# Kernel optimization log

Measured on AMD Instinct MI355X. Metric: run time of the kernel, lower is better.

The kernel has to match this reference:

```python
import jax, jax.numpy as jnp
import numpy as np

N_NODES = 50000
N_EDGES = 800000
D_IN = 128
HIDDEN = 128
N_GRAPHS = 64


def gcn_conv(x, src, dst, W, b, num_nodes):
    """PyG GCNConv: out = D^{-1/2} (A+I) D^{-1/2} (x W) + b.
    src/dst already include self-loops."""
    h = x @ W  # [N, out]
    deg = jax.ops.segment_sum(jnp.ones_like(dst, dtype=h.dtype), dst,
                              num_segments=num_nodes)  # in-degree incl. self loop
    dinv = jnp.where(deg > 0, jax.lax.rsqrt(jnp.maximum(deg, 1e-12)), 0.0)
    norm = dinv[src] * dinv[dst]  # [E+N]
    msgs = h[src] * norm[:, None]  # gather + scale
    out = jax.ops.segment_sum(msgs, dst, num_segments=num_nodes)
    return out + b


def setup_inputs() -> dict:
    key = jax.random.key(0)
    ks = jax.random.split(key, 8)
    x = jax.random.normal(ks[0], (N_NODES, D_IN), dtype=jnp.float32)
    edge_index = jax.random.randint(ks[1], (2, N_EDGES), 0, N_NODES, dtype=jnp.int64)
    batch = jnp.sort(jax.random.randint(ks[2], (N_NODES,), 0, N_GRAPHS, dtype=jnp.int64))
    # Glorot-ish scaled params
    s = lambda fan_in: 1.0 / np.sqrt(fan_in)
    W1 = jax.random.normal(ks[3], (D_IN, HIDDEN), dtype=jnp.float32) * s(D_IN)
    b1 = jnp.zeros((HIDDEN,), dtype=jnp.float32)
    W2 = jax.random.normal(ks[4], (HIDDEN, HIDDEN), dtype=jnp.float32) * s(HIDDEN)
    b2 = jnp.zeros((HIDDEN,), dtype=jnp.float32)
    Wh1 = jax.random.normal(ks[5], (HIDDEN, HIDDEN), dtype=jnp.float32) * s(HIDDEN)
    bh1 = jnp.zeros((HIDDEN,), dtype=jnp.float32)
    Wh2 = jax.random.normal(ks[6], (HIDDEN, 1), dtype=jnp.float32) * s(HIDDEN)
    bh2 = jnp.zeros((1,), dtype=jnp.float32)
    return {"x": x, "edge_index": edge_index, "batch": batch,
            "W1": W1, "b1": b1, "W2": W2, "b2": b2,
            "Wh1": Wh1, "bh1": bh1, "Wh2": Wh2, "bh2": bh2}


def reference(x, edge_index, batch, W1, b1, W2, b2, Wh1, bh1, Wh2, bh2):
    n = x.shape[0]
    loop = jnp.arange(n, dtype=edge_index.dtype)
    src = jnp.concatenate([edge_index[0], loop])  # add self-loops once
    dst = jnp.concatenate([edge_index[1], loop])
    h = jax.nn.relu(gcn_conv(x, src, dst, W1, b1, n))
    h = jax.nn.relu(gcn_conv(h, src, dst, W2, b2, n))
    # global mean pool over graphs
    sums = jax.ops.segment_sum(h, batch, num_segments=N_GRAPHS)
    cnts = jax.ops.segment_sum(jnp.ones((n,), dtype=h.dtype), batch,
                               num_segments=N_GRAPHS)
    pooled = sums / jnp.maximum(cnts, 1.0)[:, None]  # [G, HIDDEN]
    # MLP head: Linear -> ReLU -> Linear -> Sigmoid -> squeeze(-1)
    z = jax.nn.relu(pooled @ Wh1 + bh1)
    out = jax.nn.sigmoid(z @ Wh2 + bh2)
    return out[:, 0]  # [G]
```

## Files before the change

kernel.cpp:

```cpp
#include <hip/hip_runtime.h>


#define NB 256
#define NBK 256

typedef __attribute__((ext_vector_type(8))) short bf16x8;
typedef __attribute__((ext_vector_type(4))) float f32x4;
typedef __attribute__((ext_vector_type(2))) float f32x2;

__device__ inline unsigned short f2bf(float f) {
    union { float f; unsigned int u; } c; c.f = f;
    unsigned int u = c.u + (0x7fffu + ((c.u >> 16) & 1u));
    return (unsigned short)(u >> 16);
}
__device__ inline float bf2f(unsigned short b) {
    union { unsigned int u; float f; } c; c.u = ((unsigned int)b) << 16;
    return c.f;
}

__device__ inline unsigned char f2fp8_sw(float f) {
    union { float f; unsigned int u; } c; c.f = f;
    unsigned int s = (c.u >> 24) & 0x80u;
    unsigned int au = c.u & 0x7FFFFFFFu;
    if (au >= 0x3C800000u) {
        if (au > 0x43E00000u) au = 0x43E00000u;
        unsigned int r = au + 0x000FFFFFu + ((au >> 20) & 1u);
        unsigned int e8 = (r >> 23) - 120u;
        unsigned int m8 = (r >> 20) & 7u;
        return (unsigned char)(s | (e8 << 3) | m8);
    }
    float av = c.f < 0.f ? -c.f : c.f;
    unsigned int M = (unsigned int)(av * 512.0f + 0.5f);
    return (unsigned char)(s | M);
}
__device__ inline float fp82f_sw(unsigned int cbyte) {
    unsigned int E = (cbyte >> 3) & 0xFu, M = cbyte & 7u;
    union { unsigned int u; float f; } v;
    v.u = ((E + 120u) << 23) | (M << 20);
    float r = E ? v.f : (float)M * 0.001953125f;
    return (cbyte & 0x80u) ? -r : r;
}

__device__ inline f32x2 fp8x2_f32(unsigned int u) {
#if __has_builtin(__builtin_amdgcn_cvt_pk_f32_fp8)
    return __builtin_amdgcn_cvt_pk_f32_fp8(u, false);
#else
    f32x2 r; r[0] = fp82f_sw(u & 0xFFu); r[1] = fp82f_sw((u >> 8) & 0xFFu);
    return r;
#endif
}
__device__ inline unsigned char f2fp8(float f) {
#if __has_builtin(__builtin_amdgcn_cvt_pk_fp8_f32)
    return (unsigned char)(__builtin_amdgcn_cvt_pk_fp8_f32(f, f, 0, false) & 0xFFu);
#else
    return f2fp8_sw(f);
#endif
}

__global__ __launch_bounds__(256) void k_hist(const int* __restrict__ dst,
                                              int* __restrict__ hist,
                                              float* __restrict__ sums,
                                              float* __restrict__ cnt,
                                              int ne, int chunk) {
    __shared__ int h[NBK];
    int t = threadIdx.x, b = blockIdx.x;
    h[t] = 0;
    int gid = b * 256 + t;
    if (gid < 64 * 128) sums[gid] = 0.0f;
    if (gid < 64) cnt[gid] = 0.0f;
    __syncthreads();
    int e0 = b * chunk, e1 = min(e0 + chunk, ne);
    for (int e = e0 + t; e < e1; e += 256) atomicAdd(&h[dst[e] >> 8], 1);
    __syncthreads();
    hist[b * NBK + t] = h[t];
}

__global__ __launch_bounds__(256) void k_scanb(int* __restrict__ hist,
                                               int* __restrict__ bstart,
                                               int* __restrict__ row_start,
                                               int n, int ne) {
    __shared__ int ps[256];
    int j = threadIdx.x;
    int run = 0;
    for (int i = 0; i < NB; ++i) {
        int t = hist[i * NBK + j];
        hist[i * NBK + j] = run;
        run += t;
    }
    ps[j] = run;
    __syncthreads();
    for (int off = 1; off < 256; off <<= 1) {
        int v = (j >= off) ? ps[j - off] : 0;
        __syncthreads();
        ps[j] += v;
        __syncthreads();
    }
    int excl = ps[j] - run;
    bstart[j] = excl;
    if (j == 255) bstart[256] = ps[255];
    if (j == 0) row_start[n] = ne;
    for (int i = 0; i < NB; ++i) hist[i * NBK + j] += excl;
}

__global__ __launch_bounds__(256) void k_scat(const int* __restrict__ src,
                                              const int* __restrict__ dst,
                                              const int* __restrict__ hist,
                                              unsigned int* __restrict__ ebuf,
                                              int ne, int chunk) {
    __shared__ int cur[NBK];
    int t = threadIdx.x, b = blockIdx.x;
    cur[t] = hist[b * NBK + t];
    __syncthreads();
    int e0 = b * chunk, e1 = min(e0 + chunk, ne);
    for (int e = e0 + t; e < e1; e += 256) {
        int d = dst[e];
        int p = atomicAdd(&cur[d >> 8], 1);
        ebuf[p] = ((unsigned int)(d & 255) << 24) | (unsigned int)src[e];
    }
}

__global__ __launch_bounds__(256) void k_bsort(const unsigned int* __restrict__ ebuf,
                                               const int* __restrict__ bstart,
                                               int* __restrict__ csr,
                                               int* __restrict__ row_start,
                                               float* __restrict__ dinv,
                                               int n) {
    __shared__ int h[NBK];
    __shared__ int sc[NBK];
    int j = threadIdx.x, b = blockIdx.x;
    int s0 = bstart[b], s1 = bstart[b + 1];
    h[j] = 0;
    __syncthreads();
    for (int e = s0 + j; e < s1; e += 256) atomicAdd(&h[ebuf[e] >> 24], 1);
    __syncthreads();
    sc[j] = h[j];
    __syncthreads();
    for (int off = 1; off < 256; off <<= 1) {
        int v = (j >= off) ? sc[j - off] : 0;
        __syncthreads();
        sc[j] += v;
        __syncthreads();
    }
    int excl = sc[j] - h[j];
    int id = b * 256 + j;
    int deg = h[j];
    if (id < n) {
        row_start[id] = s0 + excl;
        dinv[id] = rsqrtf((float)deg + 1.0f);
    }
    __syncthreads();
    h[j] = excl;
    __syncthreads();
    for (int e = s0 + j; e < s1; e += 256) {
        unsigned int pk = ebuf[e];
        int p = atomicAdd(&h[pk >> 24], 1);
        csr[s0 + p] = (int)(pk & 0x00FFFFFFu);
    }
}

__global__ __launch_bounds__(256) void k_castw(const float* __restrict__ W1,
                                               const float* __restrict__ W2,
                                               unsigned short* __restrict__ Wt1,
                                               unsigned short* __restrict__ Wt2) {
    int tid = blockIdx.x * 256 + threadIdx.x;
    int i = tid & 16383;
    int nn = i >> 7, kk = i & 127;
    if (tid < 16384) Wt1[i] = f2bf(W1[kk * 128 + nn]);
    else             Wt2[i] = f2bf(W2[kk * 128 + nn]);
}

template <bool F32IN>
__global__ __launch_bounds__(256) void k_gemm_mfma(const void* __restrict__ Xin,
                                                   const short* __restrict__ Wt,
                                                   unsigned char* __restrict__ Y8,
                                                   int n_rows) {
    int wid = threadIdx.x >> 6;
    int lane = threadIdx.x & 63;
    int r = lane & 15, q = lane >> 4;
    int m0 = blockIdx.x * 64;
    int n0 = wid * 32;

    bf16x8 bfr[2][4];
#pragma unroll
    for (int nt = 0; nt < 2; ++nt)
#pragma unroll
        for (int ks = 0; ks < 4; ++ks)
            bfr[nt][ks] = *(const bf16x8*)(Wt + (size_t)(n0 + nt * 16 + r) * 128 +
                                           ks * 32 + q * 8);

#pragma unroll
    for (int rt = 0; rt < 4; ++rt) {
        int row = m0 + rt * 16 + r;
        int rl = min(row, n_rows - 1);
        f32x4 acc0 = {0.f, 0.f, 0.f, 0.f};
        f32x4 acc1 = {0.f, 0.f, 0.f, 0.f};
#pragma unroll
        for (int ks = 0; ks < 4; ++ks) {
            bf16x8 a;
            if constexpr (F32IN) {
                const float* xr = (const float*)Xin + (size_t)rl * 128 + ks * 32 + q * 8;
                float4 f0 = *(const float4*)xr;
                float4 f1 = *(const float4*)(xr + 4);
                a[0] = (short)f2bf(f0.x); a[1] = (short)f2bf(f0.y);
                a[2] = (short)f2bf(f0.z); a[3] = (short)f2bf(f0.w);
                a[4] = (short)f2bf(f1.x); a[5] = (short)f2bf(f1.y);
                a[6] = (short)f2bf(f1.z); a[7] = (short)f2bf(f1.w);
            } else {
                a = *(const bf16x8*)((const short*)Xin + (size_t)rl * 128 + ks * 32 + q * 8);
            }
            acc0 = __builtin_amdgcn_mfma_f32_16x16x32_bf16(a, bfr[0][ks], acc0, 0, 0, 0);
            acc1 = __builtin_amdgcn_mfma_f32_16x16x32_bf16(a, bfr[1][ks], acc1, 0, 0, 0);
        }
#pragma unroll
        for (int v = 0; v < 4; ++v) {
            int orow = m0 + rt * 16 + q * 4 + v;
            if (orow < n_rows) {
                Y8[(size_t)orow * 128 + n0 + r]      = f2fp8(acc0[v]);
                Y8[(size_t)orow * 128 + n0 + 16 + r] = f2fp8(acc1[v]);
            }
        }
    }
}

__global__ __launch_bounds__(256) void k_agg(const unsigned char* __restrict__ h8,
                                             const float* __restrict__ dinv,
                                             const int* __restrict__ csr,
                                             const int* __restrict__ row_start,
                                             const float* __restrict__ bias,
                                             unsigned short* __restrict__ out,
                                             int n) {
    int node = blockIdx.x * 4 + (threadIdx.x >> 6);
    if (node >= n) return;
    int lane = threadIdx.x & 63;
    const unsigned short* h2 = (const unsigned short*)h8;

    float di = dinv[node];

    f32x2 hv = fp8x2_f32(h2[(size_t)node * 64 + lane]);
    float ax = hv[0] * di * di;
    float ay = hv[1] * di * di;

    int beg = row_start[node];
    int end = row_start[node + 1];
    int deg = end - beg;

    int mysrc = (lane < deg) ? csr[beg + lane] : 0;
    float myw = ((lane < deg) ? dinv[mysrc] : 0.0f) * di;

    int m = min(deg, 64);
    int e = 0;
    for (; e + 4 <= m; e += 4) {
        int s0 = __shfl(mysrc, e);
        int s1 = __shfl(mysrc, e + 1);
        int s2 = __shfl(mysrc, e + 2);
        int s3 = __shfl(mysrc, e + 3);
        float w0 = __shfl(myw, e);
        float w1 = __shfl(myw, e + 1);
        float w2 = __shfl(myw, e + 2);
        float w3 = __shfl(myw, e + 3);
        unsigned int u0 = h2[(size_t)s0 * 64 + lane];
        unsigned int u1 = h2[(size_t)s1 * 64 + lane];
        unsigned int u2 = h2[(size_t)s2 * 64 + lane];
        unsigned int u3 = h2[(size_t)s3 * 64 + lane];
        f32x2 v0 = fp8x2_f32(u0);
        f32x2 v1 = fp8x2_f32(u1);
        f32x2 v2 = fp8x2_f32(u2);
        f32x2 v3 = fp8x2_f32(u3);
        ax += v0[0] * w0;  ay += v0[1] * w0;
        ax += v1[0] * w1;  ay += v1[1] * w1;
        ax += v2[0] * w2;  ay += v2[1] * w2;
        ax += v3[0] * w3;  ay += v3[1] * w3;
    }
    for (; e < m; ++e) {
        int s = __shfl(mysrc, e);
        float w = __shfl(myw, e);
        f32x2 v = fp8x2_f32(h2[(size_t)s * 64 + lane]);
        ax += v[0] * w;
        ay += v[1] * w;
    }
    for (int j = beg + 64; j < end; ++j) {
        int s = csr[j];
        float w = dinv[s] * di;
        f32x2 v = fp8x2_f32(h2[(size_t)s * 64 + lane]);
        ax += v[0] * w;
        ay += v[1] * w;
    }

    float2 bv = ((const float2*)bias)[lane];
    float ox = fmaxf(ax + bv.x, 0.0f);
    float oy = fmaxf(ay + bv.y, 0.0f);
    unsigned int pack = (unsigned int)f2bf(ox) | ((unsigned int)f2bf(oy) << 16);
    ((unsigned int*)out)[(size_t)node * 64 + lane] = pack;
}

#define POOL_CHUNK 64
__global__ __launch_bounds__(128) void k_pool(const unsigned short* __restrict__ h,
                                              const int* __restrict__ batch,
                                              float* __restrict__ sums,
                                              float* __restrict__ cnt, int n) {
    int d = threadIdx.x;
    int c0 = blockIdx.x * POOL_CHUNK;
    if (c0 >= n) return;
    int c1 = min(c0 + POOL_CHUNK, n);
    float acc = 0.f, cc = 0.f;
    int g_cur = batch[c0];
    for (int i = c0; i < c1; ++i) {
        int g = batch[i];
        if (g != g_cur) {
            atomicAdd(&sums[g_cur * 128 + d], acc);
            if (d == 0) atomicAdd(&cnt[g_cur], cc);
            acc = 0.f; cc = 0.f; g_cur = g;
        }
        acc += bf2f(h[(size_t)i * 128 + d]);
        cc += 1.f;
    }
    atomicAdd(&sums[g_cur * 128 + d], acc);
    if (d == 0) atomicAdd(&cnt[g_cur], cc);
}

__global__ __launch_bounds__(128) void k_head(const float* __restrict__ sums,
                                              const float* __restrict__ cnt,
                                              const float* __restrict__ Wh1,
                                              const float* __restrict__ bh1,
                                              const float* __restrict__ Wh2,
                                              const float* __restrict__ bh2,
                                              float* __restrict__ out) {
    int g = blockIdx.x;
    int d = threadIdx.x;
    __shared__ float sp[128];
    __shared__ float red[128];
    float c = fmaxf(cnt[g], 1.0f);
    sp[d] = sums[g * 128 + d] / c;
    __syncthreads();
    float acc = bh1[d];
    for (int k = 0; k < 128; ++k) acc += sp[k] * Wh1[k * 128 + d];
    float z = fmaxf(acc, 0.f);
    red[d] = z * Wh2[d];
    __syncthreads();
    for (int off = 64; off > 0; off >>= 1) {
        if (d < off) red[d] += red[d + off];
        __syncthreads();
    }
    if (d == 0) out[g] = 1.f / (1.f + expf(-(red[0] + bh2[0])));
}

extern "C" void kernel_launch(void* const* d_in, const int* in_sizes, int n_in,
                              void* d_out, int out_size, void* d_ws,
                              size_t ws_size, hipStream_t stream) {
    const float* x    = (const float*)d_in[0];
    const int*   ei   = (const int*)d_in[1];
    const int*   batch= (const int*)d_in[2];
    const float* W1   = (const float*)d_in[3];
    const float* b1   = (const float*)d_in[4];
    const float* W2   = (const float*)d_in[5];
    const float* b2   = (const float*)d_in[6];
    const float* Wh1  = (const float*)d_in[7];
    const float* bh1  = (const float*)d_in[8];
    const float* Wh2  = (const float*)d_in[9];
    const float* bh2  = (const float*)d_in[10];
    float* out = (float*)d_out;

    const int n  = in_sizes[0] / 128;
    const int ne = in_sizes[1] / 2;
    const int* src = ei;
    const int* dst = ei + ne;

    char* p = (char*)d_ws;
    int* hist      = (int*)p;  p += (size_t)NB * NBK * 4;
    int* bstart    = (int*)p;  p += 257 * 4;
    int* row_start = (int*)p;  p += (size_t)(n + 1) * 4;
    float* dinv    = (float*)p; p += (size_t)n * 4;
    unsigned int* ebuf = (unsigned int*)p; p += (size_t)ne * 4;
    int* csr       = (int*)p;  p += (size_t)ne * 4;
    p = (char*)(((uintptr_t)p + 15) & ~(uintptr_t)15);
    unsigned short* Wt1 = (unsigned short*)p; p += 128 * 128 * 2;
    unsigned short* Wt2 = (unsigned short*)p; p += 128 * 128 * 2;
    unsigned char* h8   = (unsigned char*)p; p += (size_t)n * 128;
    p = (char*)(((uintptr_t)p + 15) & ~(uintptr_t)15);
    unsigned short* abf = (unsigned short*)p; p += (size_t)n * 128 * 2;
    p = (char*)(((uintptr_t)p + 15) & ~(uintptr_t)15);
    float* sums = (float*)p;   p += (size_t)64 * 128 * 4;
    float* cnt  = (float*)p;

    int chunk = (ne + NB - 1) / NB;
    int nb_g = (n + 63) / 64;
    int nb_a = (n + 3) / 4;
    int nb_p = (n + POOL_CHUNK - 1) / POOL_CHUNK;

    k_hist<<<NB, 256, 0, stream>>>(dst, hist, sums, cnt, ne, chunk);
    k_scanb<<<1, 256, 0, stream>>>(hist, bstart, row_start, n, ne);
    k_scat<<<NB, 256, 0, stream>>>(src, dst, hist, ebuf, ne, chunk);
    k_bsort<<<256, 256, 0, stream>>>(ebuf, bstart, csr, row_start, dinv, n);

    k_castw<<<128, 256, 0, stream>>>(W1, W2, Wt1, Wt2);

    k_gemm_mfma<true><<<nb_g, 256, 0, stream>>>((const void*)x, (const short*)Wt1, h8, n);
    k_agg<<<nb_a, 256, 0, stream>>>(h8, dinv, csr, row_start, b1, abf, n);

    k_gemm_mfma<false><<<nb_g, 256, 0, stream>>>((const void*)abf, (const short*)Wt2, h8, n);
    k_agg<<<nb_a, 256, 0, stream>>>(h8, dinv, csr, row_start, b2, abf, n);

    k_pool<<<nb_p, 128, 0, stream>>>(abf, batch, sums, cnt, n);
    k_head<<<64, 128, 0, stream>>>(sums, cnt, Wh1, bh1, Wh2, bh2, out);
}
```

Measured before the change: 188.3 us.

## Split fp8 features into two column planes and aggregate each plane separately

The GEMM now writes its fp8 output as two 64-column planes of N×64 bytes instead of row-major N×128. Aggregation runs once per plane, so each pass gathers over a working set half the size, which is meant to fit better in cache. Within a pass, each wavefront processes four edges at once, with 16 lanes per edge each loading 4 bytes, and the partial sums are reduced across lanes with shuffles. The cost is twice as many aggregation launches, a second read of the CSR index data, and extra shuffle and reduction work.

```diff
diff --git a/kernel.cpp b/kernel.cpp
--- a/kernel.cpp
+++ b/kernel.cpp
@@ -41,11 +41,13 @@
     return (cbyte & 0x80u) ? -r : r;
 }
 
+template <bool HI>
 __device__ inline f32x2 fp8x2_f32(unsigned int u) {
 #if __has_builtin(__builtin_amdgcn_cvt_pk_f32_fp8)
-    return __builtin_amdgcn_cvt_pk_f32_fp8(u, false);
+    return __builtin_amdgcn_cvt_pk_f32_fp8(u, HI);
 #else
-    f32x2 r; r[0] = fp82f_sw(u & 0xFFu); r[1] = fp82f_sw((u >> 8) & 0xFFu);
+    unsigned int w = HI ? (u >> 16) : u;
+    f32x2 r; r[0] = fp82f_sw(w & 0xFFu); r[1] = fp82f_sw((w >> 8) & 0xFFu);
     return r;
 #endif
 }
@@ -179,6 +181,8 @@
     int r = lane & 15, q = lane >> 4;
     int m0 = blockIdx.x * 64;
     int n0 = wid * 32;
+    unsigned char* Yp = Y8 + (size_t)(n0 >> 6) * n_rows * 64;
+    int c0 = n0 & 63;
 
     bf16x8 bfr[2][4];
 #pragma unroll
@@ -215,30 +219,33 @@
         for (int v = 0; v < 4; ++v) {
             int orow = m0 + rt * 16 + q * 4 + v;
             if (orow < n_rows) {
-                Y8[(size_t)orow * 128 + n0 + r]      = f2fp8(acc0[v]);
-                Y8[(size_t)orow * 128 + n0 + 16 + r] = f2fp8(acc1[v]);
+                Yp[(size_t)orow * 64 + c0 + r]      = f2fp8(acc0[v]);
+                Yp[(size_t)orow * 64 + c0 + 16 + r] = f2fp8(acc1[v]);
             }
         }
     }
 }
 
-__global__ __launch_bounds__(256) void k_agg(const unsigned char* __restrict__ h8,
-                                             const float* __restrict__ dinv,
-                                             const int* __restrict__ csr,
-                                             const int* __restrict__ row_start,
-                                             const float* __restrict__ bias,
-                                             unsigned short* __restrict__ out,
-                                             int n) {
+__global__ __launch_bounds__(256) void k_aggp(const unsigned char* __restrict__ plane,
+                                              const float* __restrict__ dinv,
+                                              const int* __restrict__ csr,
+                                              const int* __restrict__ row_start,
+                                              const float* __restrict__ bias_ph,
+                                              unsigned short* __restrict__ out,
+                                              int n, int phofs) {
     int node = blockIdx.x * 4 + (threadIdx.x >> 6);
     if (node >= n) return;
     int lane = threadIdx.x & 63;
-    const unsigned short* h2 = (const unsigned short*)h8;
+    int slot = lane >> 4, fi = lane & 15;
+    const unsigned int* hp = (const unsigned int*)plane;
 
     float di = dinv[node];
-
-    f32x2 hv = fp8x2_f32(h2[(size_t)node * 64 + lane]);
-    float ax = hv[0] * di * di;
-    float ay = hv[1] * di * di;
+    float selfw = (slot == 0) ? di * di : 0.0f;
+    unsigned int hu = hp[(size_t)node * 16 + fi];
+    f32x2 p0 = fp8x2_f32<false>(hu);
+    f32x2 p1 = fp8x2_f32<true>(hu);
+    float a0 = p0[0] * selfw, a1 = p0[1] * selfw;
+    float a2 = p1[0] * selfw, a3 = p1[1] * selfw;
 
     int beg = row_start[node];
     int end = row_start[node + 1];
@@ -249,48 +256,54 @@
 
     int m = min(deg, 64);
     int e = 0;
-    for (; e + 4 <= m; e += 4) {
-        int s0 = __shfl(mysrc, e);
-        int s1 = __shfl(mysrc, e + 1);
-        int s2 = __shfl(mysrc, e + 2);
-        int s3 = __shfl(mysrc, e + 3);
-        float w0 = __shfl(myw, e);
-        float w1 = __shfl(myw, e + 1);
-        float w2 = __shfl(myw, e + 2);
-        float w3 = __shfl(myw, e + 3);
-        unsigned int u0 = h2[(size_t)s0 * 64 + lane];
-        unsigned int u1 = h2[(size_t)s1 * 64 + lane];
-        unsigned int u2 = h2[(size_t)s2 * 64 + lane];
-        unsigned int u3 = h2[(size_t)s3 * 64 + lane];
-        f32x2 v0 = fp8x2_f32(u0);
-        f32x2 v1 = fp8x2_f32(u1);
-        f32x2 v2 = fp8x2_f32(u2);
-        f32x2 v3 = fp8x2_f32(u3);
-        ax += v0[0] * w0;  ay += v0[1] * w0;
-        ax += v1[0] * w1;  ay += v1[1] * w1;
-        ax += v2[0] * w2;  ay += v2[1] * w2;
-        ax += v3[0] * w3;  ay += v3[1] * w3;
-    }
-    for (; e < m; ++e) {
-        int s = __shfl(mysrc, e);
-        float w = __shfl(myw, e);
-        f32x2 v = fp8x2_f32(h2[(size_t)s * 64 + lane]);
-        ax += v[0] * w;
-        ay += v[1] * w;
-    }
-    for (int j = beg + 64; j < end; ++j) {
-        int s = csr[j];
-        float w = dinv[s] * di;
-        f32x2 v = fp8x2_f32(h2[(size_t)s * 64 + lane]);
-        ax += v[0] * w;
-        ay += v[1] * w;
-    }
-
-    float2 bv = ((const float2*)bias)[lane];
-    float ox = fmaxf(ax + bv.x, 0.0f);
-    float oy = fmaxf(ay + bv.y, 0.0f);
-    unsigned int pack = (unsigned int)f2bf(ox) | ((unsigned int)f2bf(oy) << 16);
-    ((unsigned int*)out)[(size_t)node * 64 + lane] = pack;
+    for (; e + 8 <= m; e += 8) {
+        int i0 = e + slot, i1 = e + 4 + slot;
+        int s0 = __shfl(mysrc, i0);
+        int s1 = __shfl(mysrc, i1);
+        float w0 = __shfl(myw, i0);
+        float w1 = __shfl(myw, i1);
+        unsigned int u0 = hp[(size_t)s0 * 16 + fi];
+        unsigned int u1 = hp[(size_t)s1 * 16 + fi];
+        f32x2 v00 = fp8x2_f32<false>(u0), v01 = fp8x2_f32<true>(u0);
+        f32x2 v10 = fp8x2_f32<false>(u1), v11 = fp8x2_f32<true>(u1);
+        a0 += v00[0] * w0; a1 += v00[1] * w0; a2 += v01[0] * w0; a3 += v01[1] * w0;
+        a0 += v10[0] * w1; a1 += v10[1] * w1; a2 += v11[0] * w1; a3 += v11[1] * w1;
+    }
+    for (; e < m; e += 4) {
+        int idx = e + slot;
+        int s = __shfl(mysrc, idx & 63);
+        float w = __shfl(myw, idx & 63);
+        if (idx >= m) { s = 0; w = 0.0f; }
+        unsigned int u = hp[(size_t)s * 16 + fi];
+        f32x2 v0 = fp8x2_f32<false>(u), v1 = fp8x2_f32<true>(u);
+        a0 += v0[0] * w; a1 += v0[1] * w; a2 += v1[0] * w; a3 += v1[1] * w;
+    }
+    if (slot == 0) {
+        for (int j = beg + 64; j < end; ++j) {
+            int s = csr[j];
+            float w = dinv[s] * di;
+            unsigned int u = hp[(size_t)s * 16 + fi];
+            f32x2 v0 = fp8x2_f32<false>(u), v1 = fp8x2_f32<true>(u);
+            a0 += v0[0] * w; a1 += v0[1] * w; a2 += v1[0] * w; a3 += v1[1] * w;
+        }
+    }
+
+    a0 += __shfl_xor(a0, 16); a0 += __shfl_xor(a0, 32);
+    a1 += __shfl_xor(a1, 16); a1 += __shfl_xor(a1, 32);
+    a2 += __shfl_xor(a2, 16); a2 += __shfl_xor(a2, 32);
+    a3 += __shfl_xor(a3, 16); a3 += __shfl_xor(a3, 32);
+
+    if (slot == 0) {
+        float4 bv = ((const float4*)bias_ph)[fi];
+        float o0 = fmaxf(a0 + bv.x, 0.0f);
+        float o1 = fmaxf(a1 + bv.y, 0.0f);
+        float o2 = fmaxf(a2 + bv.z, 0.0f);
+        float o3 = fmaxf(a3 + bv.w, 0.0f);
+        uint2 pk;
+        pk.x = (unsigned int)f2bf(o0) | ((unsigned int)f2bf(o1) << 16);
+        pk.y = (unsigned int)f2bf(o2) | ((unsigned int)f2bf(o3) << 16);
+        *(uint2*)(out + (size_t)node * 128 + phofs + fi * 4) = pk;
+    }
 }
 
 #define POOL_CHUNK 64
@@ -386,6 +399,7 @@
     int nb_g = (n + 63) / 64;
     int nb_a = (n + 3) / 4;
     int nb_p = (n + POOL_CHUNK - 1) / POOL_CHUNK;
+    size_t plane = (size_t)n * 64;
 
     k_hist<<<NB, 256, 0, stream>>>(dst, hist, sums, cnt, ne, chunk);
     k_scanb<<<1, 256, 0, stream>>>(hist, bstart, row_start, n, ne);
@@ -395,10 +409,12 @@
     k_castw<<<128, 256, 0, stream>>>(W1, W2, Wt1, Wt2);
 
     k_gemm_mfma<true><<<nb_g, 256, 0, stream>>>((const void*)x, (const short*)Wt1, h8, n);
-    k_agg<<<nb_a, 256, 0, stream>>>(h8, dinv, csr, row_start, b1, abf, n);
+    k_aggp<<<nb_a, 256, 0, stream>>>(h8,         dinv, csr, row_start, b1,      abf, n, 0);
+    k_aggp<<<nb_a, 256, 0, stream>>>(h8 + plane, dinv, csr, row_start, b1 + 64, abf, n, 64);
 
     k_gemm_mfma<false><<<nb_g, 256, 0, stream>>>((const void*)abf, (const short*)Wt2, h8, n);
-    k_agg<<<nb_a, 256, 0, stream>>>(h8, dinv, csr, row_start, b2, abf, n);
+    k_aggp<<<nb_a, 256, 0, stream>>>(h8,         dinv, csr, row_start, b2,      abf, n, 0);
+    k_aggp<<<nb_a, 256, 0, stream>>>(h8 + plane, dinv, csr, row_start, b2 + 64, abf, n, 64);
 
     k_pool<<<nb_p, 128, 0, stream>>>(abf, batch, sums, cnt, n);
     k_head<<<64, 128, 0, stream>>>(sums, cnt, Wh1, bh1, Wh2, bh2, out);
```

New measurement: 212.7 us. +13.0%, slower.
